# Kernel tuning notes

Measured on AMD Instinct MI355X. Metric: run time of the kernel, lower is better.

Reference implementation:

```python
import jax, jax.numpy as jnp
import numpy as np

DT = 1e-3            # norse default integration step
TAU_MEM_INV = 50.0   # 1 / tau_mem, tau_mem = 0.02 from config
TAU_SYN_INV = 200.0  # norse default
V_TH = 1.0           # config['threshold']
ALPHA = 100.0        # SuperSpike surrogate sharpness (norse default)


@jax.custom_vjp
def spike(x):
    # Heaviside forward, SuperSpike surrogate gradient backward
    return (x > 0).astype(x.dtype)

def _spike_fwd(x):
    return (x > 0).astype(x.dtype), x

def _spike_bwd(res, g):
    return (g / (ALPHA * jnp.abs(res) + 1.0) ** 2,)

spike.defvjp(_spike_fwd, _spike_bwd)


def lif_step(v, i, inp):
    # norse lif_feed_forward_step: decay v and i, spike, reset, inject input into i
    v_dec = v + DT * TAU_MEM_INV * (-v + i)   # v_leak = 0
    i_dec = i - DT * TAU_SYN_INV * i
    s = spike(v_dec - V_TH)
    v_new = (1.0 - s) * v_dec                 # v_reset = 0
    i_new = i_dec + inp
    return s, v_new, i_new


def setup_inputs() -> dict:
    key = jax.random.key(0)
    ks = jax.random.split(key, 7)
    B, T, H, OUT = 256, 32, 1024, 10
    IN = 2 * 34 * 34  # 2312
    x = jax.random.uniform(ks[0], (B, T, 2, 34, 34), dtype=jnp.float32)
    s_in = 1.0 / np.sqrt(IN)
    s_h = 1.0 / np.sqrt(H)
    W1 = jax.random.uniform(ks[1], (H, IN), jnp.float32, -s_in, s_in)
    b1 = jax.random.uniform(ks[2], (H,), jnp.float32, -s_in, s_in)
    W2 = jax.random.uniform(ks[3], (H, H), jnp.float32, -s_h, s_h)
    b2 = jax.random.uniform(ks[4], (H,), jnp.float32, -s_h, s_h)
    Wout = jax.random.uniform(ks[5], (OUT, H), jnp.float32, -s_h, s_h)
    bout = jax.random.uniform(ks[6], (OUT,), jnp.float32, -s_h, s_h)
    return {"x": x, "W1": W1, "b1": b1, "W2": W2, "b2": b2, "Wout": Wout, "bout": bout}


def reference(x, W1, b1, W2, b2, Wout, bout):
    B, T = x.shape[0], x.shape[1]
    xt = x.reshape(B, T, -1).transpose(1, 0, 2)  # (T, B, IN): permute + flatten
    H, OUT = W1.shape[0], Wout.shape[0]
    zH = jnp.zeros((B, H), x.dtype)
    zO = jnp.zeros((B, OUT), x.dtype)
    carry0 = (zH, zH, zH, zH, zO, zO)  # (v1, i1, v2, i2, v_out, i_out)

    def step(carry, x_t):
        v1, i1, v2, i2, vo, io = carry
        s1, v1, i1 = lif_step(v1, i1, x_t @ W1.T + b1)
        s2, v2, i2 = lif_step(v2, i2, s1 @ W2.T + b2)
        so, vo, io = lif_step(vo, io, s2 @ Wout.T + bout)
        return (v1, i1, v2, i2, vo, io), so

    _, spikes = jax.lax.scan(step, carry0, xt)  # (T, B, OUT)
    return spikes.sum(axis=0)  # rate decoding -> (B, OUT)
```

## Files before the change

kernel.cpp:

```cpp
#include <hip/hip_runtime.h>


#define TB 256
#define TT 32
#define TH 1024
#define TIN 2312
#define TOUT 10
#define TM (TT * TB)
#define NK1 74
#define NK2 32

typedef _Float16 f16_t;
typedef f16_t f16x8 __attribute__((ext_vector_type(8)));
typedef float floatx4 __attribute__((ext_vector_type(4)));

__device__ __forceinline__ void split2h(float v, f16_t& a, f16_t& b) {
  a = (f16_t)v;
  b = (f16_t)(v - (float)a);
}

__global__ __launch_bounds__(256) void split_w_frag(
    const float* __restrict__ W, f16_t* __restrict__ P, long plane,
    int K, int nk32) {
  const int fid = blockIdx.x * 4 + (threadIdx.x >> 6);
  const int lane = threadIdx.x & 63;
  const int n16 = fid / nk32, k32 = fid - n16 * nk32;
  const long row = n16 * 16 + (lane & 15);
  const int k0 = k32 * 32 + (lane >> 4) * 8;
  float t[8];
  if (k0 + 8 <= K) {
    float4 v0 = *(const float4*)(W + row * K + k0);
    float4 v1 = *(const float4*)(W + row * K + k0 + 4);
    t[0] = v0.x; t[1] = v0.y; t[2] = v0.z; t[3] = v0.w;
    t[4] = v1.x; t[5] = v1.y; t[6] = v1.z; t[7] = v1.w;
  } else {
    #pragma unroll
    for (int e = 0; e < 8; ++e) t[e] = 0.f;
  }
  f16x8 h0, h1;
  #pragma unroll
  for (int e = 0; e < 8; ++e) {
    f16_t a, b;
    split2h(t[e], a, b);
    h0[e] = a; h1[e] = b;
  }
  const long o = (long)fid * 512 + lane * 8;
  *(f16x8*)(P + o) = h0;
  *(f16x8*)(P + plane + o) = h1;
}

__global__ __launch_bounds__(256, 2) void snn_gemm1(
    const float* __restrict__ Af, long sT, long sB,
    const f16_t* __restrict__ Bf, long planeB, int nk32, int K,
    const float* __restrict__ bias, float* __restrict__ C, int N) {
  constexpr int LDW = 36;
  __shared__ f16_t As[2][128 * LDW];

  const int tid = threadIdx.x;
  const int wave = tid >> 6, lane = tid & 63;
  const int quad = lane >> 4, l16 = lane & 15;
  const int wm = (wave & 1) * 64, wn = (wave >> 1) * 64;
  const int mblk = blockIdx.x >> 3, nblk = blockIdx.x & 7;
  const long m0 = (long)mblk * 128, n0 = (long)nblk * 128;

  floatx4 acc[4][4];
  #pragma unroll
  for (int i = 0; i < 4; ++i)
    #pragma unroll
    for (int j = 0; j < 4; ++j) acc[i][j] = (floatx4){0.f, 0.f, 0.f, 0.f};

  const int cr = tid >> 1;
  const int cs = (tid & 1) * 16;
  float4 xv[4];

  const f16_t* Bw = Bf + (((n0 + wn) >> 4) * (long)nk32) * 512 + lane * 8;

  auto prefetchA = [&](int kb) {
    const long rA = m0 + cr;
    const int k0 = kb + cs;
    const float* xr = Af + (rA >> 8) * sT + (rA & 255) * sB + k0;
    #pragma unroll
    for (int u = 0; u < 4; ++u)
      xv[u] = (k0 + u * 4 < K) ? *(const float4*)(xr + u * 4)
                               : float4{0.f, 0.f, 0.f, 0.f};
  };

  auto commitA = [&]() {
    const int off = cr * LDW + cs;
    #pragma unroll
    for (int h = 0; h < 2; ++h) {
      float t[8] = {xv[2 * h].x,     xv[2 * h].y,     xv[2 * h].z,
                    xv[2 * h].w,     xv[2 * h + 1].x, xv[2 * h + 1].y,
                    xv[2 * h + 1].z, xv[2 * h + 1].w};
      f16x8 a8, b8;
      #pragma unroll
      for (int e = 0; e < 8; ++e) {
        f16_t a, b;
        split2h(t[e], a, b);
        a8[e] = a; b8[e] = b;
      }
      *(f16x8*)(&As[0][off + h * 8]) = a8;
      *(f16x8*)(&As[1][off + h * 8]) = b8;
    }
  };

  auto loadB = [&](int k32, f16x8 (&bf)[2][4]) {
    #pragma unroll
    for (int q = 0; q < 2; ++q)
      #pragma unroll
      for (int j = 0; j < 4; ++j)
        bf[q][j] = *(const f16x8*)(Bw + q * planeB +
                                   ((long)j * nk32 + k32) * 512);
  };

  f16x8 b0[2][4], b1[2][4];
  prefetchA(0);
  loadB(0, b0);

  auto body = [&](int kt, f16x8 (&bc)[2][4], f16x8 (&bn)[2][4]) {
    __syncthreads();
    commitA();
    prefetchA(kt + 1 < nk32 ? (kt + 1) * 32 : 0);
    __syncthreads();
    loadB(kt + 1 < nk32 ? kt + 1 : 0, bn);

    f16x8 afr[2][4];
    #pragma unroll
    for (int pa = 0; pa < 2; ++pa)
      #pragma unroll
      for (int i = 0; i < 4; ++i)
        afr[pa][i] =
            *(const f16x8*)(&As[pa][(wm + i * 16 + l16) * LDW + quad * 8]);

    #pragma unroll
    for (int pb = 0; pb < 2; ++pb) {
      const int pamax = 1 - pb;
      #pragma unroll
      for (int pa = 0; pa < 2; ++pa) {
        if (pa > pamax) break;
        #pragma unroll
        for (int i = 0; i < 4; ++i)
          #pragma unroll
          for (int j = 0; j < 4; ++j)
            acc[i][j] = __builtin_amdgcn_mfma_f32_16x16x32_f16(
                afr[pa][i], bc[pb][j], acc[i][j], 0, 0, 0);
      }
    }
  };

  for (int kt = 0; kt < nk32; kt += 2) {
    body(kt, b0, b1);
    body(kt + 1, b1, b0);
  }

  #pragma unroll
  for (int j = 0; j < 4; ++j) {
    const long col = n0 + wn + j * 16 + l16;
    const float bvv = bias[col];
    #pragma unroll
    for (int i = 0; i < 4; ++i) {
      const long row0 = m0 + wm + i * 16 + quad * 4;
      #pragma unroll
      for (int g = 0; g < 4; ++g)
        C[(row0 + g) * (long)N + col] = acc[i][j][g] + bvv;
    }
  }
}

__global__ __launch_bounds__(256, 2) void snn_gemm2(
    const f16_t* __restrict__ Ab, long sT, long sB,
    const f16_t* __restrict__ Bf, long planeB, int nk32,
    const float* __restrict__ bias, float* __restrict__ C, int N) {
  constexpr int LDW = 36;
  __shared__ f16_t As[128 * LDW];

  const int tid = threadIdx.x;
  const int wave = tid >> 6, lane = tid & 63;
  const int quad = lane >> 4, l16 = lane & 15;
  const int wm = (wave & 1) * 64, wn = (wave >> 1) * 64;
  const int mblk = blockIdx.x >> 3, nblk = blockIdx.x & 7;
  const long m0 = (long)mblk * 128, n0 = (long)nblk * 128;

  floatx4 acc[4][4];
  #pragma unroll
  for (int i = 0; i < 4; ++i)
    #pragma unroll
    for (int j = 0; j < 4; ++j) acc[i][j] = (floatx4){0.f, 0.f, 0.f, 0.f};

  const int cr = tid >> 1;
  const int cs = (tid & 1) * 16;
  f16x8 av[2];

  const f16_t* Bw = Bf + (((n0 + wn) >> 4) * (long)nk32) * 512 + lane * 8;

  auto prefetchA = [&](int kb) {
    const long rA = m0 + cr;
    const f16_t* ar = Ab + (rA >> 8) * sT + (rA & 255) * sB + kb + cs;
    av[0] = *(const f16x8*)ar;
    av[1] = *(const f16x8*)(ar + 8);
  };

  auto commitA = [&]() {
    const int off = cr * LDW + cs;
    *(f16x8*)(&As[off]) = av[0];
    *(f16x8*)(&As[off + 8]) = av[1];
  };

  auto loadB = [&](int k32, f16x8 (&bf)[2][4]) {
    #pragma unroll
    for (int q = 0; q < 2; ++q)
      #pragma unroll
      for (int j = 0; j < 4; ++j)
        bf[q][j] = *(const f16x8*)(Bw + q * planeB +
                                   ((long)j * nk32 + k32) * 512);
  };

  f16x8 b0[2][4], b1[2][4];
  prefetchA(0);
  loadB(0, b0);

  auto body = [&](int kt, f16x8 (&bc)[2][4], f16x8 (&bn)[2][4]) {
    __syncthreads();
    commitA();
    prefetchA(kt + 1 < nk32 ? (kt + 1) * 32 : 0);
    __syncthreads();
    loadB(kt + 1 < nk32 ? kt + 1 : 0, bn);

    f16x8 afr[4];
    #pragma unroll
    for (int i = 0; i < 4; ++i)
      afr[i] = *(const f16x8*)(&As[(wm + i * 16 + l16) * LDW + quad * 8]);

    #pragma unroll
    for (int pb = 0; pb < 2; ++pb)
      #pragma unroll
      for (int i = 0; i < 4; ++i)
        #pragma unroll
        for (int j = 0; j < 4; ++j)
          acc[i][j] = __builtin_amdgcn_mfma_f32_16x16x32_f16(
              afr[i], bc[pb][j], acc[i][j], 0, 0, 0);
  };

  for (int kt = 0; kt < nk32; kt += 2) {
    body(kt, b0, b1);
    body(kt + 1, b1, b0);
  }

  #pragma unroll
  for (int j = 0; j < 4; ++j) {
    const long col = n0 + wn + j * 16 + l16;
    const float bvv = bias[col];
    #pragma unroll
    for (int i = 0; i < 4; ++i) {
      const long row0 = m0 + wm + i * 16 + quad * 4;
      #pragma unroll
      for (int g = 0; g < 4; ++g)
        C[(row0 + g) * (long)N + col] = acc[i][j][g] + bvv;
    }
  }
}

__global__ __launch_bounds__(256) void lif_scan_f16(const float* __restrict__ I,
                                                    f16_t* __restrict__ S) {
  int idx = blockIdx.x * 256 + threadIdx.x;
  float v = 0.f, cur = 0.f;
  #pragma unroll
  for (int t = 0; t < TT; ++t) {
    float inp = I[(long)t * (TB * TH) + idx];
    float vd = fmaf(0.05f, cur - v, v);
    float id = cur - 0.2f * cur;
    float s = (vd > 1.0f) ? 1.0f : 0.f;
    v = (1.0f - s) * vd;
    cur = id + inp;
    S[(long)t * (TB * TH) + idx] = (f16_t)s;
  }
}

__global__ __launch_bounds__(256) void gemm3_kernel(
    const f16_t* __restrict__ S2, const float* __restrict__ Wout,
    const float* __restrict__ bout, float* __restrict__ I3) {
  int wv = (blockIdx.x * blockDim.x + threadIdx.x) >> 6;
  int lane = threadIdx.x & 63;
  if (wv >= TM) return;
  const f16_t* srow = S2 + (long)wv * TH;
  float acc[TOUT];
  #pragma unroll
  for (int o = 0; o < TOUT; ++o) acc[o] = 0.f;
  for (int k = lane; k < TH; k += 64) {
    float s = (float)srow[k];
    #pragma unroll
    for (int o = 0; o < TOUT; ++o) acc[o] = fmaf(s, Wout[o * TH + k], acc[o]);
  }
  #pragma unroll
  for (int off = 32; off > 0; off >>= 1)
    #pragma unroll
    for (int o = 0; o < TOUT; ++o) acc[o] += __shfl_down(acc[o], off, 64);
  if (lane == 0) {
    #pragma unroll
    for (int o = 0; o < TOUT; ++o) I3[(long)wv * TOUT + o] = acc[o] + bout[o];
  }
}

__global__ __launch_bounds__(256) void scan_out(const float* __restrict__ I3,
                                                float* __restrict__ out) {
  int idx = blockIdx.x * blockDim.x + threadIdx.x;
  if (idx >= TB * TOUT) return;
  float v = 0.f, cur = 0.f, cnt = 0.f;
  #pragma unroll
  for (int t = 0; t < TT; ++t) {
    float inp = I3[(long)t * (TB * TOUT) + idx];
    float vd = fmaf(0.05f, cur - v, v);
    float id = cur - 0.2f * cur;
    float s = (vd > 1.0f) ? 1.0f : 0.f;
    v = (1.0f - s) * vd;
    cur = id + inp;
    cnt += s;
  }
  out[idx] = cnt;
}

extern "C" void kernel_launch(void* const* d_in, const int* in_sizes, int n_in,
                              void* d_out, int out_size, void* d_ws,
                              size_t ws_size, hipStream_t stream) {
  const float* x    = (const float*)d_in[0];
  const float* W1   = (const float*)d_in[1];
  const float* b1   = (const float*)d_in[2];
  const float* W2   = (const float*)d_in[3];
  const float* b2   = (const float*)d_in[4];
  const float* Wout = (const float*)d_in[5];
  const float* bout = (const float*)d_in[6];

  const long PL1 = 64L * NK1 * 512;
  const long PL2 = 64L * NK2 * 512;

  char* base = (char*)d_ws;
  const long S2_BYTES = (long)TM * TH * 2;
  f16_t* W1p  = (f16_t*)base;
  f16_t* W2p  = (f16_t*)(base + 2 * PL1 * 2);
  float* bufI = (float*)(base + S2_BYTES);
  f16_t* S1   = (f16_t*)(base + S2_BYTES + (long)TM * TH * 4);
  float* buf3 = (float*)(base + S2_BYTES + (long)TM * TH * 4 + (long)TM * TH * 2);
  f16_t* S2   = (f16_t*)base;

  split_w_frag<<<64 * NK1 / 4, 256, 0, stream>>>(W1, W1p, PL1, TIN, NK1);
  split_w_frag<<<64 * NK2 / 4, 256, 0, stream>>>(W2, W2p, PL2, TH, NK2);

  snn_gemm1<<<512, 256, 0, stream>>>(x, (long)TIN, (long)TT * TIN, W1p, PL1,
                                     NK1, TIN, b1, bufI, TH);

  lif_scan_f16<<<(TB * TH) / 256, 256, 0, stream>>>(bufI, S1);

  snn_gemm2<<<512, 256, 0, stream>>>(S1, (long)TB * TH, (long)TH, W2p, PL2,
                                     NK2, b2, bufI, TH);

  lif_scan_f16<<<(TB * TH) / 256, 256, 0, stream>>>(bufI, S2);

  gemm3_kernel<<<(TM * 64) / 256, 256, 0, stream>>>(S2, Wout, bout, buf3);

  scan_out<<<(TB * TOUT + 255) / 256, 256, 0, stream>>>(buf3, (float*)d_out);
}
```

Baseline: 350.8 us.

## Stage weight fragments in LDS via global_load_lds with double-buffered A/B tiles

Both GEMM kernels now load B weight fragments cooperatively into shared memory using the direct global-to-LDS load instruction, instead of each wave reading its own fragments into registers. A tiles are stored in MFMA fragment order and double-buffered, which drops one barrier per k-step. The aim is to cut redundant global traffic for B (the two waves sharing a column previously both loaded it), lower register pressure, and overlap loads with MFMA work. The cost is more LDS per block, which may reduce occupancy, plus reliance on correct ordering of the async LDS loads relative to the single barrier per iteration.

```diff
diff --git a/kernel.cpp b/kernel.cpp
--- a/kernel.cpp
+++ b/kernel.cpp
@@ -9,6 +9,7 @@
 #define TM (TT * TB)
 #define NK1 74
 #define NK2 32
+#define FR 512
 
 typedef _Float16 f16_t;
 typedef f16_t f16x8 __attribute__((ext_vector_type(8)));
@@ -17,6 +18,12 @@
 __device__ __forceinline__ void split2h(float v, f16_t& a, f16_t& b) {
   a = (f16_t)v;
   b = (f16_t)(v - (float)a);
+}
+
+__device__ __forceinline__ void gload16(const void* g, void* l) {
+  __builtin_amdgcn_global_load_lds(
+      (const __attribute__((address_space(1))) void*)g,
+      (__attribute__((address_space(3))) void*)l, 16, 0, 0);
 }
 
 __global__ __launch_bounds__(256) void split_w_frag(
@@ -53,13 +60,14 @@
     const float* __restrict__ Af, long sT, long sB,
     const f16_t* __restrict__ Bf, long planeB, int nk32, int K,
     const float* __restrict__ bias, float* __restrict__ C, int N) {
-  constexpr int LDW = 36;
-  __shared__ f16_t As[2][128 * LDW];
+  __shared__ f16_t As[2 * 2 * 8 * FR];
+  __shared__ f16_t Bs[2 * 2 * 8 * FR];
 
   const int tid = threadIdx.x;
   const int wave = tid >> 6, lane = tid & 63;
   const int quad = lane >> 4, l16 = lane & 15;
   const int wm = (wave & 1) * 64, wn = (wave >> 1) * 64;
+  const int a16 = (wave & 1) * 4, b16 = (wave >> 1) * 4;
   const int mblk = blockIdx.x >> 3, nblk = blockIdx.x & 7;
   const long m0 = (long)mblk * 128, n0 = (long)nblk * 128;
 
@@ -69,71 +77,79 @@
     #pragma unroll
     for (int j = 0; j < 4; ++j) acc[i][j] = (floatx4){0.f, 0.f, 0.f, 0.f};
 
-  const int cr = tid >> 1;
-  const int cs = (tid & 1) * 16;
+  const int cr = tid >> 1, ch = tid & 1;
+  const int am16 = cr >> 4;
+  const int lnA0 = (cr & 15) | ((2 * ch) << 4);
+  const int lnA1 = (cr & 15) | ((2 * ch + 1) << 4);
   float4 xv[4];
-
-  const f16_t* Bw = Bf + (((n0 + wn) >> 4) * (long)nk32) * 512 + lane * 8;
-
-  auto prefetchA = [&](int kb) {
-    const long rA = m0 + cr;
-    const int k0 = kb + cs;
-    const float* xr = Af + (rA >> 8) * sT + (rA & 255) * sB + k0;
+  const float* xrow = Af + ((m0 + cr) >> 8) * sT + ((m0 + cr) & 255) * sB;
+
+  auto prefetchA = [&](int kt) {
+    const int k0 = kt * 32 + ch * 16;
     #pragma unroll
     for (int u = 0; u < 4; ++u)
-      xv[u] = (k0 + u * 4 < K) ? *(const float4*)(xr + u * 4)
+      xv[u] = (k0 + u * 4 < K) ? *(const float4*)(xrow + k0 + u * 4)
                                : float4{0.f, 0.f, 0.f, 0.f};
   };
 
-  auto commitA = [&]() {
-    const int off = cr * LDW + cs;
-    #pragma unroll
-    for (int h = 0; h < 2; ++h) {
-      float t[8] = {xv[2 * h].x,     xv[2 * h].y,     xv[2 * h].z,
-                    xv[2 * h].w,     xv[2 * h + 1].x, xv[2 * h + 1].y,
-                    xv[2 * h + 1].z, xv[2 * h + 1].w};
-      f16x8 a8, b8;
+  auto commitA = [&](int buf) {
+    #pragma unroll
+    for (int half = 0; half < 2; ++half) {
+      const float* p = (const float*)&xv[half * 2];
+      f16x8 p0, p1;
       #pragma unroll
       for (int e = 0; e < 8; ++e) {
         f16_t a, b;
-        split2h(t[e], a, b);
-        a8[e] = a; b8[e] = b;
+        split2h(p[e], a, b);
+        p0[e] = a; p1[e] = b;
       }
-      *(f16x8*)(&As[0][off + h * 8]) = a8;
-      *(f16x8*)(&As[1][off + h * 8]) = b8;
-    }
-  };
-
-  auto loadB = [&](int k32, f16x8 (&bf)[2][4]) {
-    #pragma unroll
-    for (int q = 0; q < 2; ++q)
+      const int ln = half ? lnA1 : lnA0;
+      *(f16x8*)(&As[((buf * 2 + 0) * 8 + am16) * FR + ln * 8]) = p0;
+      *(f16x8*)(&As[((buf * 2 + 1) * 8 + am16) * FR + ln * 8]) = p1;
+    }
+  };
+
+  const long nbase = (n0 >> 4) * (long)nk32;
+  auto gloadB = [&](int kt, int buf) {
+    #pragma unroll
+    for (int c = 0; c < 4; ++c) {
+      const int chk = wave * 4 + c;
+      const int pl = chk >> 3, n16 = chk & 7;
+      const f16_t* src = Bf + pl * planeB +
+                         (nbase + (long)n16 * nk32 + kt) * FR + lane * 8;
+      gload16(src, &Bs[((buf * 2 + pl) * 8 + n16) * FR]);
+    }
+  };
+
+  prefetchA(0);
+  gloadB(0, 0);
+  commitA(0);
+  prefetchA(1);
+  __syncthreads();
+
+  for (int kt = 0; kt < nk32; ++kt) {
+    const int cur = kt & 1;
+    if (kt + 1 < nk32) {
+      gloadB(kt + 1, cur ^ 1);
+      commitA(cur ^ 1);
+    }
+    if (kt + 2 < nk32) prefetchA(kt + 2);
+
+    f16x8 afr[2][4];
+    #pragma unroll
+    for (int pl = 0; pl < 2; ++pl)
+      #pragma unroll
+      for (int i = 0; i < 4; ++i)
+        afr[pl][i] = *(const f16x8*)(
+            &As[((cur * 2 + pl) * 8 + a16 + i) * FR + lane * 8]);
+
+    #pragma unroll
+    for (int pb = 0; pb < 2; ++pb) {
+      f16x8 bfr[4];
       #pragma unroll
       for (int j = 0; j < 4; ++j)
-        bf[q][j] = *(const f16x8*)(Bw + q * planeB +
-                                   ((long)j * nk32 + k32) * 512);
-  };
-
-  f16x8 b0[2][4], b1[2][4];
-  prefetchA(0);
-  loadB(0, b0);
-
-  auto body = [&](int kt, f16x8 (&bc)[2][4], f16x8 (&bn)[2][4]) {
-    __syncthreads();
-    commitA();
-    prefetchA(kt + 1 < nk32 ? (kt + 1) * 32 : 0);
-    __syncthreads();
-    loadB(kt + 1 < nk32 ? kt + 1 : 0, bn);
-
-    f16x8 afr[2][4];
-    #pragma unroll
-    for (int pa = 0; pa < 2; ++pa)
-      #pragma unroll
-      for (int i = 0; i < 4; ++i)
-        afr[pa][i] =
-            *(const f16x8*)(&As[pa][(wm + i * 16 + l16) * LDW + quad * 8]);
-
-    #pragma unroll
-    for (int pb = 0; pb < 2; ++pb) {
+        bfr[j] = *(const f16x8*)(
+            &Bs[((cur * 2 + pb) * 8 + b16 + j) * FR + lane * 8]);
       const int pamax = 1 - pb;
       #pragma unroll
       for (int pa = 0; pa < 2; ++pa) {
@@ -143,14 +159,10 @@
           #pragma unroll
           for (int j = 0; j < 4; ++j)
             acc[i][j] = __builtin_amdgcn_mfma_f32_16x16x32_f16(
-                afr[pa][i], bc[pb][j], acc[i][j], 0, 0, 0);
+                afr[pa][i], bfr[j], acc[i][j], 0, 0, 0);
       }
     }
-  };
-
-  for (int kt = 0; kt < nk32; kt += 2) {
-    body(kt, b0, b1);
-    body(kt + 1, b1, b0);
+    __syncthreads();
   }
 
   #pragma unroll
@@ -171,13 +183,14 @@
     const f16_t* __restrict__ Ab, long sT, long sB,
     const f16_t* __restrict__ Bf, long planeB, int nk32,
     const float* __restrict__ bias, float* __restrict__ C, int N) {
-  constexpr int LDW = 36;
-  __shared__ f16_t As[128 * LDW];
+  __shared__ f16_t As[2 * 8 * FR];
+  __shared__ f16_t Bs[2 * 2 * 8 * FR];
 
   const int tid = threadIdx.x;
   const int wave = tid >> 6, lane = tid & 63;
   const int quad = lane >> 4, l16 = lane & 15;
   const int wm = (wave & 1) * 64, wn = (wave >> 1) * 64;
+  const int a16 = (wave & 1) * 4, b16 = (wave >> 1) * 4;
   const int mblk = blockIdx.x >> 3, nblk = blockIdx.x & 7;
   const long m0 = (long)mblk * 128, n0 = (long)nblk * 128;
 
@@ -187,63 +200,70 @@
     #pragma unroll
     for (int j = 0; j < 4; ++j) acc[i][j] = (floatx4){0.f, 0.f, 0.f, 0.f};
 
-  const int cr = tid >> 1;
-  const int cs = (tid & 1) * 16;
+  const int cr = tid >> 1, ch = tid & 1;
+  const int am16 = cr >> 4;
+  const int lnA0 = (cr & 15) | ((2 * ch) << 4);
+  const int lnA1 = (cr & 15) | ((2 * ch + 1) << 4);
   f16x8 av[2];
-
-  const f16_t* Bw = Bf + (((n0 + wn) >> 4) * (long)nk32) * 512 + lane * 8;
-
-  auto prefetchA = [&](int kb) {
-    const long rA = m0 + cr;
-    const f16_t* ar = Ab + (rA >> 8) * sT + (rA & 255) * sB + kb + cs;
-    av[0] = *(const f16x8*)ar;
-    av[1] = *(const f16x8*)(ar + 8);
-  };
-
-  auto commitA = [&]() {
-    const int off = cr * LDW + cs;
-    *(f16x8*)(&As[off]) = av[0];
-    *(f16x8*)(&As[off + 8]) = av[1];
-  };
-
-  auto loadB = [&](int k32, f16x8 (&bf)[2][4]) {
-    #pragma unroll
-    for (int q = 0; q < 2; ++q)
+  const f16_t* arow = Ab + ((m0 + cr) >> 8) * sT + ((m0 + cr) & 255) * sB;
+
+  auto prefetchA = [&](int kt) {
+    const f16_t* p = arow + kt * 32 + ch * 16;
+    av[0] = *(const f16x8*)p;
+    av[1] = *(const f16x8*)(p + 8);
+  };
+
+  auto commitA = [&](int buf) {
+    *(f16x8*)(&As[(buf * 8 + am16) * FR + lnA0 * 8]) = av[0];
+    *(f16x8*)(&As[(buf * 8 + am16) * FR + lnA1 * 8]) = av[1];
+  };
+
+  const long nbase = (n0 >> 4) * (long)nk32;
+  auto gloadB = [&](int kt, int buf) {
+    #pragma unroll
+    for (int c = 0; c < 4; ++c) {
+      const int chk = wave * 4 + c;
+      const int pl = chk >> 3, n16 = chk & 7;
+      const f16_t* src = Bf + pl * planeB +
+                         (nbase + (long)n16 * nk32 + kt) * FR + lane * 8;
+      gload16(src, &Bs[((buf * 2 + pl) * 8 + n16) * FR]);
+    }
+  };
+
+  prefetchA(0);
+  gloadB(0, 0);
+  commitA(0);
+  prefetchA(1);
+  __syncthreads();
+
+  for (int kt = 0; kt < nk32; ++kt) {
+    const int cur = kt & 1;
+    if (kt + 1 < nk32) {
+      gloadB(kt + 1, cur ^ 1);
+      commitA(cur ^ 1);
+    }
+    if (kt + 2 < nk32) prefetchA(kt + 2);
+
+    f16x8 afr[4];
+    #pragma unroll
+    for (int i = 0; i < 4; ++i)
+      afr[i] = *(const f16x8*)(&As[(cur * 8 + a16 + i) * FR + lane * 8]);
+
+    #pragma unroll
+    for (int pb = 0; pb < 2; ++pb) {
+      f16x8 bfr[4];
       #pragma unroll
       for (int j = 0; j < 4; ++j)
-        bf[q][j] = *(const f16x8*)(Bw + q * planeB +
-                                   ((long)j * nk32 + k32) * 512);
-  };
-
-  f16x8 b0[2][4], b1[2][4];
-  prefetchA(0);
-  loadB(0, b0);
-
-  auto body = [&](int kt, f16x8 (&bc)[2][4], f16x8 (&bn)[2][4]) {
-    __syncthreads();
-    commitA();
-    prefetchA(kt + 1 < nk32 ? (kt + 1) * 32 : 0);
-    __syncthreads();
-    loadB(kt + 1 < nk32 ? kt + 1 : 0, bn);
-
-    f16x8 afr[4];
-    #pragma unroll
-    for (int i = 0; i < 4; ++i)
-      afr[i] = *(const f16x8*)(&As[(wm + i * 16 + l16) * LDW + quad * 8]);
-
-    #pragma unroll
-    for (int pb = 0; pb < 2; ++pb)
+        bfr[j] = *(const f16x8*)(
+            &Bs[((cur * 2 + pb) * 8 + b16 + j) * FR + lane * 8]);
       #pragma unroll
       for (int i = 0; i < 4; ++i)
         #pragma unroll
         for (int j = 0; j < 4; ++j)
           acc[i][j] = __builtin_amdgcn_mfma_f32_16x16x32_f16(
-              afr[i], bc[pb][j], acc[i][j], 0, 0, 0);
-  };
-
-  for (int kt = 0; kt < nk32; kt += 2) {
-    body(kt, b0, b1);
-    body(kt + 1, b1, b0);
+              afr[i], bfr[j], acc[i][j], 0, 0, 0);
+    }
+    __syncthreads();
   }
 
   #pragma unroll
```

After: 358.6 us. 1.02x slower.
